# Performance work log

Measured on AMD Instinct MI355X. Metric: run time of the kernel, lower is better.

## Reference

```python
import jax, jax.numpy as jnp
import numpy as np

N_NODES = 100000
N_EDGES = 300000
N_GRAPHS = 2048
IN_DIM = 38
HID = 256
LAYERS = 5
OUT_DIM = 1
BN_EPS = 1e-5


def setup_inputs() -> dict:
    key = jax.random.key(0)
    ks = jax.random.split(key, 20)
    x = jax.random.normal(ks[0], (N_NODES, IN_DIM), dtype=jnp.float32)
    edge_index = jax.random.randint(ks[1], (2, N_EDGES), 0, N_NODES, dtype=jnp.int32)
    batch = jnp.sort(jax.random.randint(ks[2], (N_NODES,), 0, N_GRAPHS, dtype=jnp.int32))
    s_in = 1.0 / np.sqrt(IN_DIM)
    s_h = 1.0 / np.sqrt(HID)
    return {
        "x": x,
        "edge_index": edge_index,
        "batch": batch,
        "Wp": jax.random.uniform(ks[3], (IN_DIM, HID), jnp.float32, -s_in, s_in),
        "bp": jnp.zeros((HID,), jnp.float32),
        "eps": jnp.zeros((LAYERS,), jnp.float32),  # train_eps=True, init 0
        "W1s": jax.random.uniform(ks[4], (LAYERS, HID, HID), jnp.float32, -s_h, s_h),
        "b1s": jnp.zeros((LAYERS, HID), jnp.float32),
        "W2s": jax.random.uniform(ks[5], (LAYERS, HID, HID), jnp.float32, -s_h, s_h),
        "b2s": jnp.zeros((LAYERS, HID), jnp.float32),
        "gammas": jnp.ones((LAYERS, HID), jnp.float32),
        "betas": jnp.zeros((LAYERS, HID), jnp.float32),
        "Wr1": jax.random.uniform(ks[6], (HID, HID), jnp.float32, -s_h, s_h),
        "br1": jnp.zeros((HID,), jnp.float32),
        "Wr2": jax.random.uniform(ks[7], (HID, OUT_DIM), jnp.float32, -s_h, s_h),
        "br2": jnp.zeros((OUT_DIM,), jnp.float32),
    }


def _forward(x, edge_index, batch, Wp, bp, eps, W1s, b1s, W2s, b2s,
             gammas, betas, Wr1, br1, Wr2, br2):
    src, dst = edge_index[0], edge_index[1]
    h = x @ Wp + bp  # [N, HID]
    for l in range(LAYERS):
        # GINConv: (1+eps)*h_i + sum_{j->i} h_j  (scatter-add over edges)
        agg = jnp.zeros_like(h).at[dst].add(h[src])
        z = (1.0 + eps[l]) * h + agg
        # 2-layer MLP
        z = jax.nn.relu(z @ W1s[l] + b1s[l]) @ W2s[l] + b2s[l]
        # BatchNorm1d (training-mode batch statistics, biased variance)
        mu = jnp.mean(z, axis=0)
        var = jnp.var(z, axis=0)
        z = (z - mu) * jax.lax.rsqrt(var + BN_EPS) * gammas[l] + betas[l]
        h = jax.nn.relu(z)  # dropout disabled (eval)
    # global mean pool over graphs
    sums = jax.ops.segment_sum(h, batch, num_segments=N_GRAPHS)
    counts = jax.ops.segment_sum(jnp.ones((h.shape[0],), h.dtype), batch,
                                 num_segments=N_GRAPHS)
    pooled = sums / jnp.maximum(counts, 1.0)[:, None]
    # readout MLP (dropout disabled)
    out = jax.nn.relu(pooled @ Wr1 + br1) @ Wr2 + br2
    return out  # [N_GRAPHS, OUT_DIM]


def reference(x, edge_index, batch, Wp, bp, eps, W1s, b1s, W2s, b2s,
              gammas, betas, Wr1, br1, Wr2, br2):
    return _forward(x, edge_index, batch, Wp, bp, eps, W1s, b1s, W2s, b2s,
                    gammas, betas, Wr1, br1, Wr2, br2)
```

## Files before the change

### kernel.cpp

```cpp
#include <hip/hip_runtime.h>

#define N_NODES 100000
#define N_EDGES 300000
#define N_GRAPHS 2048
#define IN_DIM 38
#define HID 256
#define LAYERS 5
#define BN_EPS 1e-5f

#define SCAN_CHUNK 512
#define N_CHUNKS ((N_NODES + SCAN_CHUNK - 1) / SCAN_CHUNK)

#define ROW_PAD 128

typedef unsigned short u16;
typedef unsigned int u32;
typedef __attribute__((ext_vector_type(8))) short short8;
typedef __attribute__((ext_vector_type(4))) unsigned short ushortx4;
typedef __attribute__((ext_vector_type(4))) unsigned int uintx4;
typedef __attribute__((ext_vector_type(4))) float floatx4;

__device__ __forceinline__ unsigned short bf16_rne(float f) {
    unsigned int u = __float_as_uint(f);
    unsigned int r = (u + 0x7fffu + ((u >> 16) & 1u)) >> 16;
    return (unsigned short)r;
}
__device__ __forceinline__ float uf(unsigned short b) {
    return __uint_as_float((unsigned int)b << 16);
}
__device__ __forceinline__ float unpack_pair(u32 w) {
    return uf((unsigned short)(w & 0xffffu)) + uf((unsigned short)(w >> 16));
}
__device__ __forceinline__ void split_bf16(float v, unsigned short& hi,
                                           unsigned short& lo) {
    hi = bf16_rne(v);
    float hf = __uint_as_float((unsigned int)hi << 16);
    lo = (unsigned short)(__float_as_uint(v - hf) >> 16);
}
__device__ __forceinline__ u32 pack_pair(float v) {
    unsigned short hb, lb;
    split_bf16(v, hb, lb);
    return (u32)hb | ((u32)lb << 16);
}
__device__ __forceinline__ int swz(int b) {
    return b ^ (((b >> 8) & 3) << 4) ^ (((b >> 12) & 1) << 6);
}
__device__ __forceinline__ void bn_params(const float* sums, const float* sumsq,
                                          const float* gammas,
                                          const float* betas, int c, float& sc,
                                          float& sh) {
    const float invN = 1.0f / (float)N_NODES;
    float mu = sums[c] * invN;
    float var = sumsq[c] * invN - mu * mu;
    float rs = rsqrtf(var + BN_EPS);
    float g = gammas[c];
    sc = rs * g;
    sh = betas[c] - mu * rs * g;
}

#define PROJ_CH 64
__global__ __launch_bounds__(256) void proj_kernel(
    const float* __restrict__ x, const float* __restrict__ Wp,
    const float* __restrict__ bp, u32* __restrict__ h) {
    __shared__ float xs[PROJ_CH * IN_DIM];
    int t = threadIdx.x;
    float w[IN_DIM];
#pragma unroll
    for (int k = 0; k < IN_DIM; k++) w[k] = Wp[k * HID + t];
    float b = bp[t];
    int n0 = blockIdx.x * PROJ_CH;
    int count = min(PROJ_CH, N_NODES - n0);
    int total = count * IN_DIM;
    const float* xbase = x + (size_t)n0 * IN_DIM;
    for (int i = t; i < total; i += 256) xs[i] = xbase[i];
    __syncthreads();
    for (int n = 0; n < count; n++) {
        float acc = b;
        const float* xr = &xs[n * IN_DIM];
#pragma unroll
        for (int k = 0; k < IN_DIM; k++) acc = fmaf(xr[k], w[k], acc);
        h[(size_t)(n0 + n) * 256 + t] = pack_pair(acc);
    }
}

__global__ __launch_bounds__(256) void hist_kernel(const int* __restrict__ ei,
                                                   int* __restrict__ deg) {
    int e = blockIdx.x * 256 + threadIdx.x;
    if (e < N_EDGES) atomicAdd(&deg[ei[N_EDGES + e]], 1);
}

__global__ __launch_bounds__(256) void scan1_kernel(const int* __restrict__ deg,
                                                    int* __restrict__ offs,
                                                    int* __restrict__ blocksums) {
    __shared__ int s[SCAN_CHUNK];
    int base = blockIdx.x * SCAN_CHUNK;
    int t = threadIdx.x;
    int i0 = t, i1 = t + 256;
    int g0 = base + i0, g1 = base + i1;
    int o0 = (g0 < N_NODES) ? deg[g0] : 0;
    int o1 = (g1 < N_NODES) ? deg[g1] : 0;
    s[i0] = o0;
    s[i1] = o1;
    __syncthreads();
    for (int off = 1; off < SCAN_CHUNK; off <<= 1) {
        int v0 = (i0 >= off) ? s[i0 - off] : 0;
        int v1 = (i1 >= off) ? s[i1 - off] : 0;
        __syncthreads();
        s[i0] += v0;
        s[i1] += v1;
        __syncthreads();
    }
    if (g0 < N_NODES) offs[g0] = s[i0] - o0;
    if (g1 < N_NODES) offs[g1] = s[i1] - o1;
    if (t == 0) blocksums[blockIdx.x] = s[SCAN_CHUNK - 1];
}

__global__ __launch_bounds__(256) void scan2_kernel(int* __restrict__ blocksums) {
    __shared__ int s[256];
    int t = threadIdx.x;
    int o = (t < N_CHUNKS) ? blocksums[t] : 0;
    s[t] = o;
    __syncthreads();
    for (int off = 1; off < 256; off <<= 1) {
        int v = (t >= off) ? s[t - off] : 0;
        __syncthreads();
        s[t] += v;
        __syncthreads();
    }
    if (t < N_CHUNKS) blocksums[t] = s[t] - o;
}

__global__ __launch_bounds__(256) void scan3_kernel(int* __restrict__ offs,
                                                    const int* __restrict__ blocksums,
                                                    int* __restrict__ cursor) {
    int g = blockIdx.x * 256 + threadIdx.x;
    if (g < N_NODES) {
        int v = offs[g] + blocksums[g / SCAN_CHUNK];
        offs[g] = v;
        cursor[g] = v;
    }
    if (g == 0) offs[N_NODES] = N_EDGES;
}

__global__ __launch_bounds__(256) void fill_kernel(const int* __restrict__ ei,
                                                   int* __restrict__ cursor,
                                                   int* __restrict__ csr_src) {
    int e = blockIdx.x * 256 + threadIdx.x;
    if (e < N_EDGES) {
        int src = ei[e];
        int dst = ei[N_EDGES + e];
        int pos = atomicAdd(&cursor[dst], 1);
        csr_src[pos] = src;
    }
}

__global__ __launch_bounds__(256) void packW_kernel(const float* __restrict__ W1s,
                                                    const float* __restrict__ W2s,
                                                    short8* __restrict__ Wpk8) {
    int id = blockIdx.x * 256 + threadIdx.x;
    int lane = id & 63;
    int fid = (id >> 6) & 127;
    int w = id >> 13;
    int kt = fid >> 4, nt = fid & 15;
    const float* Wsrc = (w < 5) ? W1s + (size_t)w * HID * HID
                                : W2s + (size_t)(w - 5) * HID * HID;
    int k0 = kt * 32 + ((lane >> 4) << 3);
    int n = nt * 16 + (lane & 15);
    short8 hi, lo;
#pragma unroll
    for (int e = 0; e < 8; e++) {
        float v = Wsrc[(size_t)(k0 + e) * HID + n];
        unsigned short hb, lb;
        split_bf16(v, hb, lb);
        hi[e] = (short)hb;
        lo[e] = (short)lb;
    }
    size_t base = (size_t)w * 16384;
    Wpk8[base + (size_t)((0 * 8 + kt) * 16 + nt) * 64 + lane] = hi;
    Wpk8[base + (size_t)((1 * 8 + kt) * 16 + nt) * 64 + lane] = lo;
}

__global__ __launch_bounds__(256, 4) void fused_mlp_kernel(
    const u32* __restrict__ zin, const int* __restrict__ offs,
    const int* __restrict__ csr_src, const float* __restrict__ eps, int layer,
    const float* __restrict__ psums, const float* __restrict__ psumsq,
    const float* __restrict__ pgam, const float* __restrict__ pbet, int useBN,
    const short8* __restrict__ W1m, const float* __restrict__ b1,
    const short8* __restrict__ W2m, const float* __restrict__ b2,
    u32* __restrict__ C, int M, float* __restrict__ sums,
    float* __restrict__ sumsq) {
    __shared__ char lds[32768];
    u16* Hf = (u16*)lds;
    float* cf = (float*)lds;
    int t = threadIdx.x;
    int lane = t & 63;
    int w = t >> 6;
    int m0 = blockIdx.x * 32;
    int col15 = lane & 15;
    int rgrp = lane >> 4;

    {
        float s = 1.0f + eps[layer];
        int c0 = lane * 4;
        float4 sc = make_float4(1.f, 1.f, 1.f, 1.f);
        float4 sh = make_float4(0.f, 0.f, 0.f, 0.f);
        if (useBN) {
            bn_params(psums, psumsq, pgam, pbet, c0 + 0, sc.x, sh.x);
            bn_params(psums, psumsq, pgam, pbet, c0 + 1, sc.y, sh.y);
            bn_params(psums, psumsq, pgam, pbet, c0 + 2, sc.z, sh.z);
            bn_params(psums, psumsq, pgam, pbet, c0 + 3, sc.w, sh.w);
        }
        int fb0 = ((lane >> 3) * 2 + (w >> 1)) * 1024 + ((lane >> 1) & 3) * 256 +
                  (lane & 1) * 8 + (w & 1) * 128;
        for (int g = 0; g < 8; g++) {
            int node = m0 + w * 8 + g;
            float acc[4] = {0.f, 0.f, 0.f, 0.f};
            if (node < N_NODES) {
                int beg = offs[node], end = offs[node + 1];
                uintx4 vs = *(const uintx4*)&zin[(size_t)node * 256 + c0];
                acc[0] = unpack_pair(vs[0]);
                acc[1] = unpack_pair(vs[1]);
                acc[2] = unpack_pair(vs[2]);
                acc[3] = unpack_pair(vs[3]);
                if (useBN) {
                    acc[0] = fmaxf(acc[0] * sc.x + sh.x, 0.f);
                    acc[1] = fmaxf(acc[1] * sc.y + sh.y, 0.f);
                    acc[2] = fmaxf(acc[2] * sc.z + sh.z, 0.f);
                    acc[3] = fmaxf(acc[3] * sc.w + sh.w, 0.f);
                }
                acc[0] *= s; acc[1] *= s; acc[2] *= s; acc[3] *= s;
                for (int base = beg; base < end; base += 4) {
                    int i0 = csr_src[base];
                    int i1 = (base + 1 < end) ? csr_src[base + 1] : i0;
                    int i2 = (base + 2 < end) ? csr_src[base + 2] : i0;
                    int i3 = (base + 3 < end) ? csr_src[base + 3] : i0;
                    uintx4 r0 = *(const uintx4*)&zin[(size_t)i0 * 256 + c0];
                    uintx4 r1 = *(const uintx4*)&zin[(size_t)i1 * 256 + c0];
                    uintx4 r2 = *(const uintx4*)&zin[(size_t)i2 * 256 + c0];
                    uintx4 r3 = *(const uintx4*)&zin[(size_t)i3 * 256 + c0];
#define PROC_ROW(rv)                                                   \
                    {                                                  \
                        float v0 = unpack_pair(rv[0]);                 \
                        float v1 = unpack_pair(rv[1]);                 \
                        float v2 = unpack_pair(rv[2]);                 \
                        float v3 = unpack_pair(rv[3]);                 \
                        if (useBN) {                                   \
                            v0 = fmaxf(v0 * sc.x + sh.x, 0.f);         \
                            v1 = fmaxf(v1 * sc.y + sh.y, 0.f);         \
                            v2 = fmaxf(v2 * sc.z + sh.z, 0.f);         \
                            v3 = fmaxf(v3 * sc.w + sh.w, 0.f);         \
                        }                                              \
                        acc[0] += v0; acc[1] += v1;                    \
                        acc[2] += v2; acc[3] += v3;                    \
                    }
                    PROC_ROW(r0);
                    if (base + 1 < end) PROC_ROW(r1);
                    if (base + 2 < end) PROC_ROW(r2);
                    if (base + 3 < end) PROC_ROW(r3);
#undef PROC_ROW
                }
            }
            ushortx4 ho, lo2;
#pragma unroll
            for (int q = 0; q < 4; q++) {
                unsigned short hb, lb;
                split_bf16(acc[q], hb, lb);
                ho[q] = hb;
                lo2[q] = lb;
            }
            int sb = swz(fb0 + g * 16);
            *(ushortx4*)(lds + sb) = ho;
            *(ushortx4*)(lds + sb + 16384) = lo2;
        }
    }
    __syncthreads();

    floatx4 acc[2][4];
#pragma unroll
    for (int i = 0; i < 2; i++)
#pragma unroll
        for (int j = 0; j < 4; j++) acc[i][j] = (floatx4)0.0f;

#pragma unroll
    for (int kk = 0; kk < 8; kk++) {
        short8 bb0[4], bb1[4];
#pragma unroll
        for (int j = 0; j < 4; j++) {
            bb0[j] = W1m[((size_t)(0 * 8 + kk) * 16 + (w * 4 + j)) * 64 + lane];
            bb1[j] = W1m[((size_t)(1 * 8 + kk) * 16 + (w * 4 + j)) * 64 + lane];
        }
        short8 ah[2], al[2];
#pragma unroll
        for (int mt = 0; mt < 2; mt++) {
            int ib = swz(((kk * 2 + mt) * 64 + lane) * 16);
            ah[mt] = *(short8*)(lds + ib);
            al[mt] = *(short8*)(lds + ib + 16384);
        }
        __builtin_amdgcn_s_setprio(1);
#pragma unroll
        for (int i = 0; i < 2; i++)
#pragma unroll
            for (int j = 0; j < 4; j++) {
                acc[i][j] = __builtin_amdgcn_mfma_f32_16x16x32_bf16(
                    ah[i], bb0[j], acc[i][j], 0, 0, 0);
                acc[i][j] = __builtin_amdgcn_mfma_f32_16x16x32_bf16(
                    ah[i], bb1[j], acc[i][j], 0, 0, 0);
                acc[i][j] = __builtin_amdgcn_mfma_f32_16x16x32_bf16(
                    al[i], bb0[j], acc[i][j], 0, 0, 0);
            }
        __builtin_amdgcn_s_setprio(0);
    }
    __syncthreads();

#pragma unroll
    for (int j = 0; j < 4; j++) {
        int col = w * 64 + j * 16 + col15;
        float bv = b1[col];
        int kt2 = col >> 5;
        int colg = (col & 31) >> 3;
        int e = col & 7;
#pragma unroll
        for (int i = 0; i < 2; i++) {
            int lane_a = rgrp * 4 + colg * 16;
#pragma unroll
            for (int r = 0; r < 4; r++) {
                float v = fmaxf(acc[i][j][r] + bv, 0.0f);
                unsigned short hb, lb;
                split_bf16(v, hb, lb);
                Hf[(((0 * 8 + kt2) * 2 + i) * 64 + lane_a + r) * 8 + e] = hb;
                Hf[(((1 * 8 + kt2) * 2 + i) * 64 + lane_a + r) * 8 + e] = lb;
            }
        }
    }
    __syncthreads();

    floatx4 acc2[2][4];
#pragma unroll
    for (int i = 0; i < 2; i++)
#pragma unroll
        for (int j = 0; j < 4; j++) acc2[i][j] = (floatx4)0.0f;

#pragma unroll
    for (int kj = 0; kj < 8; kj++) {
        short8 bb2[2][4];
#pragma unroll
        for (int p = 0; p < 2; p++)
#pragma unroll
            for (int j = 0; j < 4; j++)
                bb2[p][j] =
                    W2m[((size_t)(p * 8 + kj) * 16 + (w * 4 + j)) * 64 + lane];
        short8 ah2[2], al2[2];
#pragma unroll
        for (int mt = 0; mt < 2; mt++) {
            ah2[mt] = *(short8*)&Hf[(((0 * 8 + kj) * 2 + mt) * 64 + lane) * 8];
            al2[mt] = *(short8*)&Hf[(((1 * 8 + kj) * 2 + mt) * 64 + lane) * 8];
        }
        __builtin_amdgcn_s_setprio(1);
#pragma unroll
        for (int i = 0; i < 2; i++)
#pragma unroll
            for (int j = 0; j < 4; j++) {
                acc2[i][j] = __builtin_amdgcn_mfma_f32_16x16x32_bf16(
                    ah2[i], bb2[0][j], acc2[i][j], 0, 0, 0);
                acc2[i][j] = __builtin_amdgcn_mfma_f32_16x16x32_bf16(
                    ah2[i], bb2[1][j], acc2[i][j], 0, 0, 0);
                acc2[i][j] = __builtin_amdgcn_mfma_f32_16x16x32_bf16(
                    al2[i], bb2[0][j], acc2[i][j], 0, 0, 0);
            }
        __builtin_amdgcn_s_setprio(0);
    }
    __syncthreads();

#pragma unroll
    for (int j = 0; j < 4; j++) {
        int col = w * 64 + j * 16 + col15;
        float bv = b2[col];
        float csum = 0.f, csq = 0.f;
#pragma unroll
        for (int i = 0; i < 2; i++) {
            int rowb = i * 16 + rgrp * 4;
#pragma unroll
            for (int r = 0; r < 4; r++) {
                float v = acc2[i][j][r] + bv;
                cf[(rowb + r) * 256 + col] = v;
                if (m0 + rowb + r < M) {
                    csum += v;
                    csq += v * v;
                }
            }
        }
        csum += __shfl_xor(csum, 16);
        csum += __shfl_xor(csum, 32);
        csq += __shfl_xor(csq, 16);
        csq += __shfl_xor(csq, 32);
        if (rgrp == 0) {
            atomicAdd(&sums[col], csum);
            atomicAdd(&sumsq[col], csq);
        }
    }
    __syncthreads();
#pragma unroll
    for (int k = 0; k < 8; k++) {
        int fi = (k * 256 + t) * 4;
        int row = fi >> 8, colc = fi & 255;
        int m = m0 + row;
        if (m >= M) continue;
        float4 v4 = *(float4*)&cf[fi];
        uintx4 o;
        o[0] = pack_pair(v4.x);
        o[1] = pack_pair(v4.y);
        o[2] = pack_pair(v4.z);
        o[3] = pack_pair(v4.w);
        *(uintx4*)&C[(size_t)m * 256 + colc] = o;
    }
}

__global__ __launch_bounds__(256) void bounds_kernel(const int* __restrict__ batch,
                                                     int* __restrict__ start) {
    int g = blockIdx.x * 256 + threadIdx.x;
    if (g > N_GRAPHS) return;
    int lo = 0, hi = N_NODES;
    while (lo < hi) {
        int mid = (lo + hi) >> 1;
        if (batch[mid] < g) lo = mid + 1;
        else hi = mid;
    }
    start[g] = lo;
}

__global__ __launch_bounds__(256) void segpool_kernel(
    const u32* __restrict__ z, const int* __restrict__ start,
    const float* __restrict__ sums, const float* __restrict__ sumsq,
    const float* __restrict__ gammas, const float* __restrict__ betas,
    float* __restrict__ pooled) {
    int g = blockIdx.x;
    int c = threadIdx.x;
    float sc, sh;
    bn_params(sums, sumsq, gammas, betas, c, sc, sh);
    int beg = start[g], end = start[g + 1];
    float s = 0.f;
    for (int n = beg; n < end; n++) {
        float v = unpack_pair(z[(size_t)n * 256 + c]);
        s += fmaxf(v * sc + sh, 0.f);
    }
    float inv = 1.0f / fmaxf((float)(end - beg), 1.0f);
    pooled[(size_t)g * HID + c] = s * inv;
}

#define RGK 8
__global__ __launch_bounds__(256) void readout_kernel(
    const float* __restrict__ pooled, const float* __restrict__ Wr1,
    const float* __restrict__ br1, const float* __restrict__ Wr2,
    const float* __restrict__ br2, float* __restrict__ out) {
    __shared__ float p[RGK][HID];
    __shared__ float red[RGK][4];
    int g0 = blockIdx.x * RGK;
    int t = threadIdx.x;
#pragma unroll
    for (int q = 0; q < RGK; q++) p[q][t] = pooled[(size_t)(g0 + q) * HID + t];
    __syncthreads();
    int c = t;
    float acc[RGK];
#pragma unroll
    for (int q = 0; q < RGK; q++) acc[q] = br1[c];
    for (int k = 0; k < HID; k++) {
        float wv = Wr1[k * HID + c];
#pragma unroll
        for (int q = 0; q < RGK; q++) acc[q] = fmaf(p[q][k], wv, acc[q]);
    }
    float w2 = Wr2[c];
#pragma unroll
    for (int q = 0; q < RGK; q++) {
        float v = fmaxf(acc[q], 0.f) * w2;
#pragma unroll
        for (int off = 32; off > 0; off >>= 1) v += __shfl_down(v, off, 64);
        if ((c & 63) == 0) red[q][c >> 6] = v;
    }
    __syncthreads();
    if (t < RGK)
        out[g0 + t] = red[t][0] + red[t][1] + red[t][2] + red[t][3] + br2[0];
}

extern "C" void kernel_launch(void* const* d_in, const int* in_sizes, int n_in,
                              void* d_out, int out_size, void* d_ws, size_t ws_size,
                              hipStream_t stream) {
    const float* x      = (const float*)d_in[0];
    const int*   ei     = (const int*)d_in[1];
    const int*   batch  = (const int*)d_in[2];
    const float* Wp     = (const float*)d_in[3];
    const float* bp     = (const float*)d_in[4];
    const float* eps    = (const float*)d_in[5];
    const float* W1s    = (const float*)d_in[6];
    const float* b1s    = (const float*)d_in[7];
    const float* W2s    = (const float*)d_in[8];
    const float* b2s    = (const float*)d_in[9];
    const float* gammas = (const float*)d_in[10];
    const float* betas  = (const float*)d_in[11];
    const float* Wr1    = (const float*)d_in[12];
    const float* br1    = (const float*)d_in[13];
    const float* Wr2    = (const float*)d_in[14];
    const float* br2    = (const float*)d_in[15];
    float* out = (float*)d_out;

    const size_t ROWS = (size_t)N_NODES + ROW_PAD;
    u32* bufA     = (u32*)d_ws;
    u32* bufC     = bufA + ROWS * 256;
    short8* Wpk8  = (short8*)(bufC + ROWS * 256);
    float* sums   = (float*)(Wpk8 + 10 * 16384);
    float* pooled = sums + LAYERS * 512;
    int* start     = (int*)(pooled + (size_t)N_GRAPHS * HID);
    int* deg       = start + N_GRAPHS + 1;
    int* offs      = deg + N_NODES;
    int* cursor    = offs + N_NODES + 1;
    int* csr_src   = cursor + N_NODES;
    int* blocksums = csr_src + N_EDGES;

    hipMemsetAsync(deg, 0, N_NODES * sizeof(int), stream);
    hipMemsetAsync(sums, 0, LAYERS * 512 * sizeof(float), stream);
    hist_kernel<<<(N_EDGES + 255) / 256, 256, 0, stream>>>(ei, deg);
    scan1_kernel<<<N_CHUNKS, 256, 0, stream>>>(deg, offs, blocksums);
    scan2_kernel<<<1, 256, 0, stream>>>(blocksums);
    scan3_kernel<<<(N_NODES + 255) / 256, 256, 0, stream>>>(offs, blocksums,
                                                            cursor);
    fill_kernel<<<(N_EDGES + 255) / 256, 256, 0, stream>>>(ei, cursor, csr_src);
    packW_kernel<<<320, 256, 0, stream>>>(W1s, W2s, Wpk8);
    bounds_kernel<<<(N_GRAPHS + 1 + 255) / 256, 256, 0, stream>>>(batch, start);

    proj_kernel<<<(N_NODES + PROJ_CH - 1) / PROJ_CH, 256, 0, stream>>>(x, Wp, bp,
                                                                       bufA);

    const int MLP_BLOCKS = (N_NODES + 31) / 32;
    u32* zin = bufA;
    u32* zout = bufC;
    for (int l = 0; l < LAYERS; l++) {
        float* lsums = sums + l * 512;
        float* lsumsq = lsums + 256;
        const float* psums = sums + (l - 1) * 512;
        fused_mlp_kernel<<<MLP_BLOCKS, 256, 0, stream>>>(
            zin, offs, csr_src, eps, l,
            l > 0 ? psums : sums, l > 0 ? psums + 256 : sums,
            gammas + (l > 0 ? (l - 1) : 0) * HID,
            betas + (l > 0 ? (l - 1) : 0) * HID, l > 0 ? 1 : 0,
            Wpk8 + (size_t)l * 16384, b1s + l * HID,
            Wpk8 + (size_t)(5 + l) * 16384, b2s + l * HID, zout, N_NODES,
            lsums, lsumsq);
        u32* tmp = zin; zin = zout; zout = tmp;
    }

    segpool_kernel<<<N_GRAPHS, 256, 0, stream>>>(
        zin, start, sums + 4 * 512, sums + 4 * 512 + 256, gammas + 4 * HID,
        betas + 4 * HID, pooled);
    readout_kernel<<<N_GRAPHS / RGK, 256, 0, stream>>>(pooled, Wr1, br1, Wr2, br2,
                                                       out);
}
```

Before: 1.035 ms.

## Make fused GIN MLP persistent and overlap next-tile gather with GEMM2

Turns the fused gather+MLP kernel into a persistent kernel with 512 blocks that loop over 32-node tiles. The neighbour gather for the next tile is interleaved with the second GEMM's MFMA loop, and its results go into a separate LDS half. The goal is to hide the latency of the irregular gather loads behind tensor-core work. In exchange LDS doubles to 64KB and occupancy drops to 2 blocks per CU. NTILES is N_NODES/32, which divides exactly here, and the bounds check on the gather is removed.

New measurement: 3.044 ms. 194% more time.

```diff
diff --git a/kernel.cpp b/kernel.cpp
--- a/kernel.cpp
+++ b/kernel.cpp
@@ -10,6 +10,9 @@
 
 #define SCAN_CHUNK 512
 #define N_CHUNKS ((N_NODES + SCAN_CHUNK - 1) / SCAN_CHUNK)
+
+#define NTILES (N_NODES / 32)
+#define PIPE_BLOCKS 512
 
 #define ROW_PAD 128
 
@@ -180,7 +183,7 @@
     Wpk8[base + (size_t)((1 * 8 + kt) * 16 + nt) * 64 + lane] = lo;
 }
 
-__global__ __launch_bounds__(256, 4) void fused_mlp_kernel(
+__global__ __launch_bounds__(256, 2) void fused_mlp_kernel(
     const u32* __restrict__ zin, const int* __restrict__ offs,
     const int* __restrict__ csr_src, const float* __restrict__ eps, int layer,
     const float* __restrict__ psums, const float* __restrict__ psumsq,
@@ -189,229 +192,243 @@
     const short8* __restrict__ W2m, const float* __restrict__ b2,
     u32* __restrict__ C, int M, float* __restrict__ sums,
     float* __restrict__ sumsq) {
-    __shared__ char lds[32768];
-    u16* Hf = (u16*)lds;
-    float* cf = (float*)lds;
+    __shared__ char lds[65536];
+    u16* Hf = (u16*)(lds + 32768);
+    float* cf = (float*)(lds + 32768);
     int t = threadIdx.x;
     int lane = t & 63;
     int w = t >> 6;
-    int m0 = blockIdx.x * 32;
     int col15 = lane & 15;
     int rgrp = lane >> 4;
 
+    float gs = 1.0f + eps[layer];
+    int c0 = lane * 4;
+    float4 sc = make_float4(1.f, 1.f, 1.f, 1.f);
+    float4 sh = make_float4(0.f, 0.f, 0.f, 0.f);
+    if (useBN) {
+        bn_params(psums, psumsq, pgam, pbet, c0 + 0, sc.x, sh.x);
+        bn_params(psums, psumsq, pgam, pbet, c0 + 1, sc.y, sh.y);
+        bn_params(psums, psumsq, pgam, pbet, c0 + 2, sc.z, sh.z);
+        bn_params(psums, psumsq, pgam, pbet, c0 + 3, sc.w, sh.w);
+    }
+    int fb0 = ((lane >> 3) * 2 + (w >> 1)) * 1024 + ((lane >> 1) & 3) * 256 +
+              (lane & 1) * 8 + (w & 1) * 128;
+
+    auto gnode = [&](int node, int g) {
+        float acc[4] = {0.f, 0.f, 0.f, 0.f};
+        {
+            int beg = offs[node], end = offs[node + 1];
+            uintx4 vs = *(const uintx4*)&zin[(size_t)node * 256 + c0];
+            acc[0] = unpack_pair(vs[0]);
+            acc[1] = unpack_pair(vs[1]);
+            acc[2] = unpack_pair(vs[2]);
+            acc[3] = unpack_pair(vs[3]);
+            if (useBN) {
+                acc[0] = fmaxf(acc[0] * sc.x + sh.x, 0.f);
+                acc[1] = fmaxf(acc[1] * sc.y + sh.y, 0.f);
+                acc[2] = fmaxf(acc[2] * sc.z + sh.z, 0.f);
+                acc[3] = fmaxf(acc[3] * sc.w + sh.w, 0.f);
+            }
+            acc[0] *= gs; acc[1] *= gs; acc[2] *= gs; acc[3] *= gs;
+            for (int base = beg; base < end; base += 4) {
+                int i0 = csr_src[base];
+                int i1 = (base + 1 < end) ? csr_src[base + 1] : i0;
+                int i2 = (base + 2 < end) ? csr_src[base + 2] : i0;
+                int i3 = (base + 3 < end) ? csr_src[base + 3] : i0;
+                uintx4 r0 = *(const uintx4*)&zin[(size_t)i0 * 256 + c0];
+                uintx4 r1 = *(const uintx4*)&zin[(size_t)i1 * 256 + c0];
+                uintx4 r2 = *(const uintx4*)&zin[(size_t)i2 * 256 + c0];
+                uintx4 r3 = *(const uintx4*)&zin[(size_t)i3 * 256 + c0];
+#define PROC_ROW(rv)                                               \
+                {                                                  \
+                    float v0 = unpack_pair(rv[0]);                 \
+                    float v1 = unpack_pair(rv[1]);                 \
+                    float v2 = unpack_pair(rv[2]);                 \
+                    float v3 = unpack_pair(rv[3]);                 \
+                    if (useBN) {                                   \
+                        v0 = fmaxf(v0 * sc.x + sh.x, 0.f);         \
+                        v1 = fmaxf(v1 * sc.y + sh.y, 0.f);         \
+                        v2 = fmaxf(v2 * sc.z + sh.z, 0.f);         \
+                        v3 = fmaxf(v3 * sc.w + sh.w, 0.f);         \
+                    }                                              \
+                    acc[0] += v0; acc[1] += v1;                    \
+                    acc[2] += v2; acc[3] += v3;                    \
+                }
+                PROC_ROW(r0);
+                if (base + 1 < end) PROC_ROW(r1);
+                if (base + 2 < end) PROC_ROW(r2);
+                if (base + 3 < end) PROC_ROW(r3);
+#undef PROC_ROW
+            }
+        }
+        ushortx4 ho, lo2;
+#pragma unroll
+        for (int q = 0; q < 4; q++) {
+            unsigned short hb, lb;
+            split_bf16(acc[q], hb, lb);
+            ho[q] = hb;
+            lo2[q] = lb;
+        }
+        int sb = swz(fb0 + g * 16);
+        *(ushortx4*)(lds + sb) = ho;
+        *(ushortx4*)(lds + sb + 16384) = lo2;
+    };
+
+    int tile = blockIdx.x;
     {
-        float s = 1.0f + eps[layer];
-        int c0 = lane * 4;
-        float4 sc = make_float4(1.f, 1.f, 1.f, 1.f);
-        float4 sh = make_float4(0.f, 0.f, 0.f, 0.f);
-        if (useBN) {
-            bn_params(psums, psumsq, pgam, pbet, c0 + 0, sc.x, sh.x);
-            bn_params(psums, psumsq, pgam, pbet, c0 + 1, sc.y, sh.y);
-            bn_params(psums, psumsq, pgam, pbet, c0 + 2, sc.z, sh.z);
-            bn_params(psums, psumsq, pgam, pbet, c0 + 3, sc.w, sh.w);
-        }
-        int fb0 = ((lane >> 3) * 2 + (w >> 1)) * 1024 + ((lane >> 1) & 3) * 256 +
-                  (lane & 1) * 8 + (w & 1) * 128;
-        for (int g = 0; g < 8; g++) {
-            int node = m0 + w * 8 + g;
-            float acc[4] = {0.f, 0.f, 0.f, 0.f};
-            if (node < N_NODES) {
-                int beg = offs[node], end = offs[node + 1];
-                uintx4 vs = *(const uintx4*)&zin[(size_t)node * 256 + c0];
-                acc[0] = unpack_pair(vs[0]);
-                acc[1] = unpack_pair(vs[1]);
-                acc[2] = unpack_pair(vs[2]);
-                acc[3] = unpack_pair(vs[3]);
-                if (useBN) {
-                    acc[0] = fmaxf(acc[0] * sc.x + sh.x, 0.f);
-                    acc[1] = fmaxf(acc[1] * sc.y + sh.y, 0.f);
-                    acc[2] = fmaxf(acc[2] * sc.z + sh.z, 0.f);
-                    acc[3] = fmaxf(acc[3] * sc.w + sh.w, 0.f);
+        int nb = tile * 32 + w * 8;
+#pragma unroll
+        for (int g = 0; g < 8; g++) gnode(nb + g, g);
+    }
+
+    for (;;) {
+        int next = tile + PIPE_BLOCKS;
+        int hasNext = (next < NTILES);
+        int m0 = tile * 32;
+        __syncthreads();
+
+        floatx4 acc[2][4];
+#pragma unroll
+        for (int i = 0; i < 2; i++)
+#pragma unroll
+            for (int j = 0; j < 4; j++) acc[i][j] = (floatx4)0.0f;
+
+#pragma unroll
+        for (int kk = 0; kk < 8; kk++) {
+            short8 bb0[4], bb1[4];
+#pragma unroll
+            for (int j = 0; j < 4; j++) {
+                bb0[j] = W1m[((size_t)(0 * 8 + kk) * 16 + (w * 4 + j)) * 64 + lane];
+                bb1[j] = W1m[((size_t)(1 * 8 + kk) * 16 + (w * 4 + j)) * 64 + lane];
+            }
+            short8 ah[2], al[2];
+#pragma unroll
+            for (int mt = 0; mt < 2; mt++) {
+                int ib = swz(((kk * 2 + mt) * 64 + lane) * 16);
+                ah[mt] = *(short8*)(lds + ib);
+                al[mt] = *(short8*)(lds + ib + 16384);
+            }
+            __builtin_amdgcn_s_setprio(1);
+#pragma unroll
+            for (int i = 0; i < 2; i++)
+#pragma unroll
+                for (int j = 0; j < 4; j++) {
+                    acc[i][j] = __builtin_amdgcn_mfma_f32_16x16x32_bf16(
+                        ah[i], bb0[j], acc[i][j], 0, 0, 0);
+                    acc[i][j] = __builtin_amdgcn_mfma_f32_16x16x32_bf16(
+                        ah[i], bb1[j], acc[i][j], 0, 0, 0);
+                    acc[i][j] = __builtin_amdgcn_mfma_f32_16x16x32_bf16(
+                        al[i], bb0[j], acc[i][j], 0, 0, 0);
                 }
-                acc[0] *= s; acc[1] *= s; acc[2] *= s; acc[3] *= s;
-                for (int base = beg; base < end; base += 4) {
-                    int i0 = csr_src[base];
-                    int i1 = (base + 1 < end) ? csr_src[base + 1] : i0;
-                    int i2 = (base + 2 < end) ? csr_src[base + 2] : i0;
-                    int i3 = (base + 3 < end) ? csr_src[base + 3] : i0;
-                    uintx4 r0 = *(const uintx4*)&zin[(size_t)i0 * 256 + c0];
-                    uintx4 r1 = *(const uintx4*)&zin[(size_t)i1 * 256 + c0];
-                    uintx4 r2 = *(const uintx4*)&zin[(size_t)i2 * 256 + c0];
-                    uintx4 r3 = *(const uintx4*)&zin[(size_t)i3 * 256 + c0];
-#define PROC_ROW(rv)                                                   \
-                    {                                                  \
-                        float v0 = unpack_pair(rv[0]);                 \
-                        float v1 = unpack_pair(rv[1]);                 \
-                        float v2 = unpack_pair(rv[2]);                 \
-                        float v3 = unpack_pair(rv[3]);                 \
-                        if (useBN) {                                   \
-                            v0 = fmaxf(v0 * sc.x + sh.x, 0.f);         \
-                            v1 = fmaxf(v1 * sc.y + sh.y, 0.f);         \
-                            v2 = fmaxf(v2 * sc.z + sh.z, 0.f);         \
-                            v3 = fmaxf(v3 * sc.w + sh.w, 0.f);         \
-                        }                                              \
-                        acc[0] += v0; acc[1] += v1;                    \
-                        acc[2] += v2; acc[3] += v3;                    \
+            __builtin_amdgcn_s_setprio(0);
+        }
+        __syncthreads();
+
+#pragma unroll
+        for (int j = 0; j < 4; j++) {
+            int col = w * 64 + j * 16 + col15;
+            float bv = b1[col];
+            int kt2 = col >> 5;
+            int colg = (col & 31) >> 3;
+            int e = col & 7;
+#pragma unroll
+            for (int i = 0; i < 2; i++) {
+                int lane_a = rgrp * 4 + colg * 16;
+#pragma unroll
+                for (int r = 0; r < 4; r++) {
+                    float v = fmaxf(acc[i][j][r] + bv, 0.0f);
+                    unsigned short hb, lb;
+                    split_bf16(v, hb, lb);
+                    Hf[(((0 * 8 + kt2) * 2 + i) * 64 + lane_a + r) * 8 + e] = hb;
+                    Hf[(((1 * 8 + kt2) * 2 + i) * 64 + lane_a + r) * 8 + e] = lb;
+                }
+            }
+        }
+        __syncthreads();
+
+        floatx4 acc2[2][4];
+#pragma unroll
+        for (int i = 0; i < 2; i++)
+#pragma unroll
+            for (int j = 0; j < 4; j++) acc2[i][j] = (floatx4)0.0f;
+
+        int nb = next * 32 + w * 8;
+#pragma unroll
+        for (int kj = 0; kj < 8; kj++) {
+            short8 bb2[2][4];
+#pragma unroll
+            for (int p = 0; p < 2; p++)
+#pragma unroll
+                for (int j = 0; j < 4; j++)
+                    bb2[p][j] =
+                        W2m[((size_t)(p * 8 + kj) * 16 + (w * 4 + j)) * 64 + lane];
+            short8 ah2[2], al2[2];
+#pragma unroll
+            for (int mt = 0; mt < 2; mt++) {
+                ah2[mt] = *(short8*)&Hf[(((0 * 8 + kj) * 2 + mt) * 64 + lane) * 8];
+                al2[mt] = *(short8*)&Hf[(((1 * 8 + kj) * 2 + mt) * 64 + lane) * 8];
+            }
+            __builtin_amdgcn_s_setprio(1);
+#pragma unroll
+            for (int i = 0; i < 2; i++)
+#pragma unroll
+                for (int j = 0; j < 4; j++) {
+                    acc2[i][j] = __builtin_amdgcn_mfma_f32_16x16x32_bf16(
+                        ah2[i], bb2[0][j], acc2[i][j], 0, 0, 0);
+                    acc2[i][j] = __builtin_amdgcn_mfma_f32_16x16x32_bf16(
+                        ah2[i], bb2[1][j], acc2[i][j], 0, 0, 0);
+                    acc2[i][j] = __builtin_amdgcn_mfma_f32_16x16x32_bf16(
+                        al2[i], bb2[0][j], acc2[i][j], 0, 0, 0);
+                }
+            __builtin_amdgcn_s_setprio(0);
+            if (hasNext) gnode(nb + kj, kj);
+        }
+        __syncthreads();
+
+#pragma unroll
+        for (int j = 0; j < 4; j++) {
+            int col = w * 64 + j * 16 + col15;
+            float bv = b2[col];
+            float csum = 0.f, csq = 0.f;
+#pragma unroll
+            for (int i = 0; i < 2; i++) {
+                int rowb = i * 16 + rgrp * 4;
+#pragma unroll
+                for (int r = 0; r < 4; r++) {
+                    float v = acc2[i][j][r] + bv;
+                    cf[(rowb + r) * 256 + col] = v;
+                    if (m0 + rowb + r < M) {
+                        csum += v;
+                        csq += v * v;
                     }
-                    PROC_ROW(r0);
-                    if (base + 1 < end) PROC_ROW(r1);
-                    if (base + 2 < end) PROC_ROW(r2);
-                    if (base + 3 < end) PROC_ROW(r3);
-#undef PROC_ROW
                 }
             }
-            ushortx4 ho, lo2;
-#pragma unroll
-            for (int q = 0; q < 4; q++) {
-                unsigned short hb, lb;
-                split_bf16(acc[q], hb, lb);
-                ho[q] = hb;
-                lo2[q] = lb;
-            }
-            int sb = swz(fb0 + g * 16);
-            *(ushortx4*)(lds + sb) = ho;
-            *(ushortx4*)(lds + sb + 16384) = lo2;
-        }
-    }
-    __syncthreads();
-
-    floatx4 acc[2][4];
-#pragma unroll
-    for (int i = 0; i < 2; i++)
-#pragma unroll
-        for (int j = 0; j < 4; j++) acc[i][j] = (floatx4)0.0f;
-
-#pragma unroll
-    for (int kk = 0; kk < 8; kk++) {
-        short8 bb0[4], bb1[4];
-#pragma unroll
-        for (int j = 0; j < 4; j++) {
-            bb0[j] = W1m[((size_t)(0 * 8 + kk) * 16 + (w * 4 + j)) * 64 + lane];
-            bb1[j] = W1m[((size_t)(1 * 8 + kk) * 16 + (w * 4 + j)) * 64 + lane];
-        }
-        short8 ah[2], al[2];
-#pragma unroll
-        for (int mt = 0; mt < 2; mt++) {
-            int ib = swz(((kk * 2 + mt) * 64 + lane) * 16);
-            ah[mt] = *(short8*)(lds + ib);
-            al[mt] = *(short8*)(lds + ib + 16384);
-        }
-        __builtin_amdgcn_s_setprio(1);
-#pragma unroll
-        for (int i = 0; i < 2; i++)
-#pragma unroll
-            for (int j = 0; j < 4; j++) {
-                acc[i][j] = __builtin_amdgcn_mfma_f32_16x16x32_bf16(
-                    ah[i], bb0[j], acc[i][j], 0, 0, 0);
-                acc[i][j] = __builtin_amdgcn_mfma_f32_16x16x32_bf16(
-                    ah[i], bb1[j], acc[i][j], 0, 0, 0);
-                acc[i][j] = __builtin_amdgcn_mfma_f32_16x16x32_bf16(
-                    al[i], bb0[j], acc[i][j], 0, 0, 0);
-            }
-        __builtin_amdgcn_s_setprio(0);
-    }
-    __syncthreads();
-
-#pragma unroll
-    for (int j = 0; j < 4; j++) {
-        int col = w * 64 + j * 16 + col15;
-        float bv = b1[col];
-        int kt2 = col >> 5;
-        int colg = (col & 31) >> 3;
-        int e = col & 7;
-#pragma unroll
-        for (int i = 0; i < 2; i++) {
-            int lane_a = rgrp * 4 + colg * 16;
-#pragma unroll
-            for (int r = 0; r < 4; r++) {
-                float v = fmaxf(acc[i][j][r] + bv, 0.0f);
-                unsigned short hb, lb;
-                split_bf16(v, hb, lb);
-                Hf[(((0 * 8 + kt2) * 2 + i) * 64 + lane_a + r) * 8 + e] = hb;
-                Hf[(((1 * 8 + kt2) * 2 + i) * 64 + lane_a + r) * 8 + e] = lb;
-            }
-        }
-    }
-    __syncthreads();
-
-    floatx4 acc2[2][4];
-#pragma unroll
-    for (int i = 0; i < 2; i++)
-#pragma unroll
-        for (int j = 0; j < 4; j++) acc2[i][j] = (floatx4)0.0f;
-
-#pragma unroll
-    for (int kj = 0; kj < 8; kj++) {
-        short8 bb2[2][4];
-#pragma unroll
-        for (int p = 0; p < 2; p++)
-#pragma unroll
-            for (int j = 0; j < 4; j++)
-                bb2[p][j] =
-                    W2m[((size_t)(p * 8 + kj) * 16 + (w * 4 + j)) * 64 + lane];
-        short8 ah2[2], al2[2];
-#pragma unroll
-        for (int mt = 0; mt < 2; mt++) {
-            ah2[mt] = *(short8*)&Hf[(((0 * 8 + kj) * 2 + mt) * 64 + lane) * 8];
-            al2[mt] = *(short8*)&Hf[(((1 * 8 + kj) * 2 + mt) * 64 + lane) * 8];
-        }
-        __builtin_amdgcn_s_setprio(1);
-#pragma unroll
-        for (int i = 0; i < 2; i++)
-#pragma unroll
-            for (int j = 0; j < 4; j++) {
-                acc2[i][j] = __builtin_amdgcn_mfma_f32_16x16x32_bf16(
-                    ah2[i], bb2[0][j], acc2[i][j], 0, 0, 0);
-                acc2[i][j] = __builtin_amdgcn_mfma_f32_16x16x32_bf16(
-                    ah2[i], bb2[1][j], acc2[i][j], 0, 0, 0);
-                acc2[i][j] = __builtin_amdgcn_mfma_f32_16x16x32_bf16(
-                    al2[i], bb2[0][j], acc2[i][j], 0, 0, 0);
-            }
-        __builtin_amdgcn_s_setprio(0);
-    }
-    __syncthreads();
-
-#pragma unroll
-    for (int j = 0; j < 4; j++) {
-        int col = w * 64 + j * 16 + col15;
-        float bv = b2[col];
-        float csum = 0.f, csq = 0.f;
-#pragma unroll
-        for (int i = 0; i < 2; i++) {
-            int rowb = i * 16 + rgrp * 4;
-#pragma unroll
-            for (int r = 0; r < 4; r++) {
-                float v = acc2[i][j][r] + bv;
-                cf[(rowb + r) * 256 + col] = v;
-                if (m0 + rowb + r < M) {
-                    csum += v;
-                    csq += v * v;
-                }
-            }
-        }
-        csum += __shfl_xor(csum, 16);
-        csum += __shfl_xor(csum, 32);
-        csq += __shfl_xor(csq, 16);
-        csq += __shfl_xor(csq, 32);
-        if (rgrp == 0) {
-            atomicAdd(&sums[col], csum);
-            atomicAdd(&sumsq[col], csq);
-        }
-    }
-    __syncthreads();
-#pragma unroll
-    for (int k = 0; k < 8; k++) {
-        int fi = (k * 256 + t) * 4;
-        int row = fi >> 8, colc = fi & 255;
-        int m = m0 + row;
-        if (m >= M) continue;
-        float4 v4 = *(float4*)&cf[fi];
-        uintx4 o;
-        o[0] = pack_pair(v4.x);
-        o[1] = pack_pair(v4.y);
-        o[2] = pack_pair(v4.z);
-        o[3] = pack_pair(v4.w);
-        *(uintx4*)&C[(size_t)m * 256 + colc] = o;
+            csum += __shfl_xor(csum, 16);
+            csum += __shfl_xor(csum, 32);
+            csq += __shfl_xor(csq, 16);
+            csq += __shfl_xor(csq, 32);
+            if (rgrp == 0) {
+                atomicAdd(&sums[col], csum);
+                atomicAdd(&sumsq[col], csq);
+            }
+        }
+        __syncthreads();
+#pragma unroll
+        for (int k = 0; k < 8; k++) {
+            int fi = (k * 256 + t) * 4;
+            int row = fi >> 8, colc = fi & 255;
+            int m = m0 + row;
+            if (m >= M) continue;
+            float4 v4 = *(float4*)&cf[fi];
+            uintx4 o;
+            o[0] = pack_pair(v4.x);
+            o[1] = pack_pair(v4.y);
+            o[2] = pack_pair(v4.z);
+            o[3] = pack_pair(v4.w);
+            *(uintx4*)&C[(size_t)m * 256 + colc] = o;
+        }
+        if (!hasNext) break;
+        tile = next;
     }
 }
 
@@ -529,14 +546,13 @@
     proj_kernel<<<(N_NODES + PROJ_CH - 1) / PROJ_CH, 256, 0, stream>>>(x, Wp, bp,
                                                                        bufA);
 
-    const int MLP_BLOCKS = (N_NODES + 31) / 32;
     u32* zin = bufA;
     u32* zout = bufC;
     for (int l = 0; l < LAYERS; l++) {
         float* lsums = sums + l * 512;
         float* lsumsq = lsums + 256;
         const float* psums = sums + (l - 1) * 512;
-        fused_mlp_kernel<<<MLP_BLOCKS, 256, 0, stream>>>(
+        fused_mlp_kernel<<<PIPE_BLOCKS, 256, 0, stream>>>(
             zin, offs, csr_src, eps, l,
             l > 0 ? psums : sums, l > 0 ? psums + 256 : sums,
             gammas + (l > 0 ? (l - 1) : 0) * HID,
```
